# Optimization experiments

Hardware: AMD Instinct MI355X
Metric: run time of the kernel (lower is better)

Reference implementation:

```python
import jax, jax.numpy as jnp
import numpy as np

N = 2048
DIM_A = 256   # appearance feature dim (hardcoded 256 in WK/WQ/WV)
DIM_K = 64    # key_feature_dim
DIM_G = 64    # geo_feature_dim


def setup_inputs() -> dict:
    key = jax.random.key(0)
    ks = jax.random.split(key, 12)
    s = 0.05
    return {
        "f_a": jax.random.normal(ks[0], (N, DIM_A), dtype=jnp.float32),
        "position_embedding": jax.random.normal(ks[1], (N, N, DIM_G), dtype=jnp.float32),
        # torch nn.Linear weights are [out_features, in_features]
        "WG_w": jax.random.normal(ks[2], (1, DIM_G), dtype=jnp.float32) * s,
        "WG_b": jax.random.normal(ks[3], (1,), dtype=jnp.float32) * s,
        "WK_w": jax.random.normal(ks[4], (DIM_K, DIM_A), dtype=jnp.float32) * s,
        "WK_b": jax.random.normal(ks[5], (DIM_K,), dtype=jnp.float32) * s,
        "WQ_w": jax.random.normal(ks[6], (DIM_K, DIM_A), dtype=jnp.float32) * s,
        "WQ_b": jax.random.normal(ks[7], (DIM_K,), dtype=jnp.float32) * s,
        "WV_w": jax.random.normal(ks[8], (DIM_K, DIM_A), dtype=jnp.float32) * s,
        "WV_b": jax.random.normal(ks[9], (DIM_K,), dtype=jnp.float32) * s,
    }


def reference(f_a, position_embedding, WG_w, WG_b, WK_w, WK_b, WQ_w, WQ_b, WV_w, WV_b):
    n = f_a.shape[0]
    dim_k = WK_w.shape[0]
    dim_g = WG_w.shape[1]
    # geometric bias: relu(WG(g)), then log-clamp -> [N, N]
    w_g = jax.nn.relu(position_embedding.reshape(-1, dim_g) @ WG_w.T + WG_b).reshape(n, n)
    # projections of appearance features
    w_k = f_a @ WK_w.T + WK_b   # [N, dim_k]  (key index m)
    w_q = f_a @ WQ_w.T + WQ_b   # [N, dim_k]  (query index n)
    w_v = f_a @ WV_w.T + WV_b   # [N, dim_k]
    # scaled dot product: scores[m, n] = k_m . q_n / sqrt(dim_k)
    scaled_dot = (w_k @ w_q.T) / jnp.sqrt(jnp.asarray(dim_k, dtype=f_a.dtype))
    w_mn = jnp.log(jnp.clip(w_g, 1e-6)) + scaled_dot
    w_mn = jax.nn.softmax(w_mn, axis=1)        # softmax over dim=1 as in source
    # weighted sum of values along the softmax axis -> [N, dim_k]
    output = w_mn @ w_v
    return output
```

## Files before the change

### kernel.cpp

```cpp
#include <hip/hip_runtime.h>
#include <hip/hip_bf16.h>
#include <math.h>

#define NN 2048
#define DA 256
#define DK 64
#define DG 64

typedef float f32x4 __attribute__((ext_vector_type(4)));

__device__ __forceinline__ float wave_reduce_max(float v) {
  #pragma unroll
  for (int o = 32; o >= 1; o >>= 1) v = fmaxf(v, __shfl_xor(v, o, 64));
  return v;
}
__device__ __forceinline__ float wave_reduce_sum(float v) {
  #pragma unroll
  for (int o = 32; o >= 1; o >>= 1) v += __shfl_xor(v, o, 64);
  return v;
}

__device__ __forceinline__ float dpp_reduce16(float x) {
  int t;
  t = __builtin_amdgcn_update_dpp(0, __float_as_int(x), 0xB1, 0xF, 0xF, true);
  x += __int_as_float(t);
  t = __builtin_amdgcn_update_dpp(0, __float_as_int(x), 0x4E, 0xF, 0xF, true);
  x += __int_as_float(t);
  t = __builtin_amdgcn_update_dpp(0, __float_as_int(x), 0x124, 0xF, 0xF, true);
  x += __int_as_float(t);
  t = __builtin_amdgcn_update_dpp(0, __float_as_int(x), 0x128, 0xF, 0xF, true);
  x += __int_as_float(t);
  return x;
}

__device__ __forceinline__ float dot4(const f32x4 a, const f32x4 b) {
  float d = a.x * b.x;
  d = fmaf(a.y, b.y, d);
  d = fmaf(a.z, b.z, d);
  d = fmaf(a.w, b.w, d);
  return d;
}

__global__ __launch_bounds__(256) void proj_kernel(
    const float* __restrict__ fa,
    const float* __restrict__ WKw, const float* __restrict__ WKb,
    const float* __restrict__ WQw, const float* __restrict__ WQb,
    const float* __restrict__ WVw, const float* __restrict__ WVb,
    float* __restrict__ wk, float* __restrict__ wq, float* __restrict__ wv)
{
  __shared__ float s_fa[DA];
  const int m = blockIdx.x, tid = threadIdx.x;
  s_fa[tid] = fa[(size_t)m * DA + tid];
  __syncthreads();
  if (tid < 192) {
    const int o = tid >> 6, k = tid & 63;
    const float* W = (o == 0 ? WKw : (o == 1 ? WQw : WVw)) + (size_t)k * DA;
    const float* B = (o == 0 ? WKb : (o == 1 ? WQb : WVb));
    float acc = B[k];
    const float4* W4 = (const float4*)W;
    const float4* F4 = (const float4*)s_fa;
    #pragma unroll 8
    for (int c = 0; c < DA / 4; ++c) {
      float4 w4 = W4[c], f4 = F4[c];
      acc = fmaf(w4.x, f4.x, acc); acc = fmaf(w4.y, f4.y, acc);
      acc = fmaf(w4.z, f4.z, acc); acc = fmaf(w4.w, f4.w, acc);
    }
    float* dst = (o == 0 ? wk : (o == 1 ? wq : wv));
    dst[(size_t)m * DK + k] = acc;
  }
}

__global__ __launch_bounds__(256) void fused_kernel(
    const float* __restrict__ pe,
    const float* __restrict__ wgw, const float* __restrict__ wgb,
    const float* __restrict__ wk, const float* __restrict__ wq,
    const float* __restrict__ wv,
    float* __restrict__ out)
{
  __shared__ float s_logit[NN];
  __shared__ float s_rmax[4], s_rsum[4];
  __shared__ float s_pacc[4][4][DK];

  const int m = blockIdx.x, tid = threadIdx.x;
  const int wave = tid >> 6, lane = tid & 63;
  const int sub = lane >> 4;
  const int c4  = lane & 15;

  const f32x4 wg4 = ((const f32x4*)wgw)[c4];
  const f32x4 wk4 = ((const f32x4*)(wk + (size_t)m * DK))[c4];
  const float gb = wgb[0];

  float lmax = -INFINITY;
  const int n0 = wave * (NN / 4);
  #pragma unroll 4
  for (int it = 0; it < (NN / 4) / 4; ++it) {
    const int nb = n0 + it * 4;
    const f32x4 p = ((const f32x4*)(pe + ((size_t)m * NN + nb) * DG))[lane];
    const f32x4 q = ((const f32x4*)(wq + (size_t)nb * DK))[lane];
    float dg = dot4(p, wg4);
    float dq = dot4(q, wk4);
    dg = dpp_reduce16(dg);
    dq = dpp_reduce16(dq);
    if (c4 == 0) {
      const float logit = __logf(fmaxf(dg + gb, 1e-6f)) + dq * 0.125f;
      s_logit[nb + sub] = logit;
      lmax = fmaxf(lmax, logit);
    }
  }
  lmax = wave_reduce_max(lmax);
  if (lane == 0) s_rmax[wave] = lmax;
  __syncthreads();
  const float rmax = fmaxf(fmaxf(s_rmax[0], s_rmax[1]), fmaxf(s_rmax[2], s_rmax[3]));

  float lsum = 0.f;
  #pragma unroll
  for (int i = 0; i < NN / 256; ++i) {
    const int n = i * 256 + tid;
    const float p = __expf(s_logit[n] - rmax);
    s_logit[n] = p;
    lsum += p;
  }
  lsum = wave_reduce_sum(lsum);
  if (lane == 0) s_rsum[wave] = lsum;
  __syncthreads();
  const float inv = 1.0f / (s_rsum[0] + s_rsum[1] + s_rsum[2] + s_rsum[3]);

  f32x4 acc = {0.f, 0.f, 0.f, 0.f};
  #pragma unroll 4
  for (int it = 0; it < (NN / 4) / 4; ++it) {
    const int nb = n0 + it * 4;
    const float pb = s_logit[nb + sub];
    const f32x4 v = ((const f32x4*)(wv + (size_t)(nb + sub) * DK))[c4];
    acc.x = fmaf(pb, v.x, acc.x);
    acc.y = fmaf(pb, v.y, acc.y);
    acc.z = fmaf(pb, v.z, acc.z);
    acc.w = fmaf(pb, v.w, acc.w);
  }
  ((f32x4*)&s_pacc[wave][sub][0])[c4] = acc;
  __syncthreads();
  if (tid < DK) {
    float r = 0.f;
    #pragma unroll
    for (int w = 0; w < 4; ++w)
      #pragma unroll
      for (int s = 0; s < 4; ++s)
        r += s_pacc[w][s][tid];
    out[(size_t)m * DK + tid] = r * inv;
  }
}

extern "C" void kernel_launch(void* const* d_in, const int* in_sizes, int n_in,
                              void* d_out, int out_size, void* d_ws, size_t ws_size,
                              hipStream_t stream) {
  const float* fa  = (const float*)d_in[0];
  const float* pe  = (const float*)d_in[1];
  const float* wgw = (const float*)d_in[2];
  const float* wgb = (const float*)d_in[3];
  const float* wkw = (const float*)d_in[4];
  const float* wkb = (const float*)d_in[5];
  const float* wqw = (const float*)d_in[6];
  const float* wqb = (const float*)d_in[7];
  const float* wvw = (const float*)d_in[8];
  const float* wvb = (const float*)d_in[9];
  float* out = (float*)d_out;

  float* wk = (float*)d_ws;
  float* wq = wk + (size_t)NN * DK;
  float* wv = wq + (size_t)NN * DK;

  proj_kernel<<<NN, 256, 0, stream>>>(fa, wkw, wkb, wqw, wqb, wvw, wvb, wk, wq, wv);
  fused_kernel<<<NN, 256, 0, stream>>>(pe, wgw, wgb, wk, wq, wv, out);
}
```

Measured before the change: 279.2 us.

## Double-buffer position-embedding and query loads into LDS via global_load_lds

The logit loop now stages each wave's position-embedding and query rows into double-buffered LDS slices with direct global-to-LDS loads. The next chunk is prefetched while the current one is computed, with an explicit vmcnt wait and a peeled final iteration. The goal is to overlap streaming of the large position-embedding tensor with the dot products and log. The risk is that it limits each wave to one chunk in flight, where the unrolled register loads could issue more, and it adds LDS traffic.

```diff
diff --git a/kernel.cpp b/kernel.cpp
--- a/kernel.cpp
+++ b/kernel.cpp
@@ -39,6 +39,12 @@
   d = fmaf(a.z, b.z, d);
   d = fmaf(a.w, b.w, d);
   return d;
+}
+
+__device__ __forceinline__ void stage16(const float* gp, float* lp) {
+  __builtin_amdgcn_global_load_lds(
+      (const __attribute__((address_space(1))) void*)gp,
+      (__attribute__((address_space(3))) void*)lp, 16, 0, 0);
 }
 
 __global__ __launch_bounds__(256) void proj_kernel(
@@ -78,6 +84,8 @@
     float* __restrict__ out)
 {
   __shared__ float s_logit[NN];
+  __shared__ float s_pe[4][2][256];
+  __shared__ float s_q[4][2][256];
   __shared__ float s_rmax[4], s_rsum[4];
   __shared__ float s_pacc[4][4][DK];
 
@@ -89,21 +97,45 @@
   const f32x4 wg4 = ((const f32x4*)wgw)[c4];
   const f32x4 wk4 = ((const f32x4*)(wk + (size_t)m * DK))[c4];
   const float gb = wgb[0];
+  const int n0 = wave * (NN / 4);
+
+  const float* pew = pe + ((size_t)m * NN + n0) * DG;
+  const float* qw  = wq + (size_t)n0 * DK;
 
   float lmax = -INFINITY;
-  const int n0 = wave * (NN / 4);
-  #pragma unroll 4
-  for (int it = 0; it < (NN / 4) / 4; ++it) {
-    const int nb = n0 + it * 4;
-    const f32x4 p = ((const f32x4*)(pe + ((size_t)m * NN + nb) * DG))[lane];
-    const f32x4 q = ((const f32x4*)(wq + (size_t)nb * DK))[lane];
+  stage16(pew + lane * 4, &s_pe[wave][0][0]);
+  stage16(qw  + lane * 4, &s_q[wave][0][0]);
+  #pragma unroll 2
+  for (int t = 0; t < 127; ++t) {
+    const int cur = t & 1, nxt = cur ^ 1;
+    stage16(pew + (size_t)(t + 1) * 256 + lane * 4, &s_pe[wave][nxt][0]);
+    stage16(qw  + (size_t)(t + 1) * 256 + lane * 4, &s_q[wave][nxt][0]);
+    asm volatile("s_waitcnt vmcnt(2)" ::: "memory");
+    __builtin_amdgcn_sched_barrier(0);
+    const f32x4 p = ((const f32x4*)&s_pe[wave][cur][0])[lane];
+    const f32x4 q = ((const f32x4*)&s_q[wave][cur][0])[lane];
     float dg = dot4(p, wg4);
     float dq = dot4(q, wk4);
     dg = dpp_reduce16(dg);
     dq = dpp_reduce16(dq);
     if (c4 == 0) {
       const float logit = __logf(fmaxf(dg + gb, 1e-6f)) + dq * 0.125f;
-      s_logit[nb + sub] = logit;
+      s_logit[n0 + t * 4 + sub] = logit;
+      lmax = fmaxf(lmax, logit);
+    }
+  }
+  asm volatile("s_waitcnt vmcnt(0)" ::: "memory");
+  __builtin_amdgcn_sched_barrier(0);
+  {
+    const f32x4 p = ((const f32x4*)&s_pe[wave][1][0])[lane];
+    const f32x4 q = ((const f32x4*)&s_q[wave][1][0])[lane];
+    float dg = dot4(p, wg4);
+    float dq = dot4(q, wk4);
+    dg = dpp_reduce16(dg);
+    dq = dpp_reduce16(dq);
+    if (c4 == 0) {
+      const float logit = __logf(fmaxf(dg + gb, 1e-6f)) + dq * 0.125f;
+      s_logit[n0 + 127 * 4 + sub] = logit;
       lmax = fmaxf(lmax, logit);
     }
   }
```

Measured after the change: 299.9 us. 1.07x slower.
